# Kernel tuning notes

Hardware: AMD Instinct MI355X
Metric: run time of the kernel (lower is better)

## Reference

```python
import jax, jax.numpy as jnp
import numpy as np

B = 4096
INPUT_SIZE = 256
OUT_WINDOW = 10
C = 16
OUTPUT_SIZE = 2  # real/imag pair
WIN = INPUT_SIZE - OUT_WINDOW + 1  # 247
BN_EPS = 1e-5


def setup_inputs() -> dict:
    key = jax.random.key(0)
    ks = jax.random.split(key, 7)
    return {
        "x": jax.random.normal(ks[0], (B, INPUT_SIZE, C, 2), dtype=jnp.float32),
        "W_in_real": jax.random.normal(ks[1], (C, WIN), dtype=jnp.float32),
        "W_in_imag": jax.random.normal(ks[2], (C, WIN), dtype=jnp.float32),
        "W_nl": jax.random.normal(ks[3], (C, OUTPUT_SIZE, 2 * (C - 1)), dtype=jnp.float32) * 0.1,
        "W_coeff": jax.random.normal(ks[4], (OUTPUT_SIZE, OUTPUT_SIZE), dtype=jnp.float32),
        "W_out_real": jax.random.normal(ks[5], (C, OUT_WINDOW), dtype=jnp.float32),
        "W_out_imag": jax.random.normal(ks[6], (C, OUT_WINDOW), dtype=jnp.float32),
        "bn_gamma": jnp.ones((C,), jnp.float32),
        "bn_beta": jnp.zeros((C,), jnp.float32),
    }


def _depthwise_filter(x_bcn, w_ck):
    # per-channel valid cross-correlation: out[b,c,w] = sum_k x[b,c,w+k] * w_ck[c,k]
    kern = w_ck[:, None, :]  # (O=C, I/groups=1, K)
    return jax.lax.conv_general_dilated(
        x_bcn, kern, window_strides=(1,), padding="VALID",
        dimension_numbers=("NCH", "OIH", "NCH"), feature_group_count=C)


def reference(x, W_in_real, W_in_imag, W_nl, W_coeff, W_out_real, W_out_imag, bn_gamma, bn_beta):
    # x: [B, N, C, 2]
    x_real = jnp.transpose(x[..., 0], (0, 2, 1))  # [B, C, N]
    x_imag = jnp.transpose(x[..., 1], (0, 2, 1))
    # unfold + per-channel FIR filter == depthwise valid correlation -> [B, W, C]
    f_r = jnp.transpose(_depthwise_filter(x_real, W_in_real), (0, 2, 1))
    f_i = jnp.transpose(_depthwise_filter(x_imag, W_in_imag), (0, 2, 1))
    # cubic amplitude nonlinearity
    amp = f_r * f_r + f_i * f_i
    f_r = amp * f_r
    f_i = amp * f_i
    # masked cross-channel gather (all channels except self), static indices
    nbr = np.stack([np.delete(np.arange(C), c) for c in range(C)])  # [C, C-1]
    nonlin_in = jnp.concatenate([f_r[:, :, nbr], f_i[:, :, nbr]], axis=-1)  # [B, W, C, 2(C-1)]
    # per-channel mixing then shared coeff mix
    nonlin_out = jnp.einsum("bwcf,cof->bwco", nonlin_in, W_nl)   # [B, W, C, 2]
    coeff_out = jnp.einsum("bwco,po->bwcp", nonlin_out, W_coeff)  # [B, W, C, 2]
    # per-channel output FIR over the out_window axis
    out_r = jnp.einsum("bwc,cw->bc", coeff_out[..., 0], W_out_real)
    out_i = jnp.einsum("bwc,cw->bc", coeff_out[..., 1], W_out_imag)
    out = jnp.stack([out_r, out_i], axis=-1)  # [B, C, 2]
    # BatchNorm1d over channel axis C (training mode, biased batch stats)
    mu = jnp.mean(out, axis=(0, 2))
    var = jnp.mean(jnp.square(out - mu[None, :, None]), axis=(0, 2))
    scale = (bn_gamma * jax.lax.rsqrt(var + BN_EPS))[None, :, None]
    return (out - mu[None, :, None]) * scale + bn_beta[None, :, None]
```

## Files before the change

### kernel.cpp

```cpp
#include <hip/hip_runtime.h>

#define BTOT 4096
#define G 8
#define NC 16
#define WIN 247
#define KPAD 250
#define WST 251
#define NW 10
#define NBLK (BTOT / G)

__global__ __launch_bounds__(256) void k_main(
    const float* __restrict__ x,
    const float* __restrict__ Wr, const float* __restrict__ Wi,
    const float* __restrict__ Wnl, const float* __restrict__ Wc,
    const float* __restrict__ Wor, const float* __restrict__ Woi,
    float* __restrict__ out, float* __restrict__ ws)
{
    __shared__ float Wlds[2 * NC * WST];
    __shared__ float fbuf[G * 32 * NW];
    __shared__ float WnlS[NC * 2 * 30];
    __shared__ float WoS[2 * 160];
    __shared__ float WcS[4];
    __shared__ float red[256];
    __shared__ float redq[128];

    float* crS = Wlds;
    float* ciS = Wlds + 1280;

    const int tid = threadIdx.x;
    const int b0 = blockIdx.x * G;

    for (int idx = tid; idx < 2 * NC * KPAD; idx += 256) {
        int ri  = idx / (NC * KPAD);
        int rem = idx - ri * (NC * KPAD);
        int c   = rem / KPAD;
        int k   = rem - c * KPAD;
        float v = 0.f;
        if (k < WIN) v = ri ? Wi[c * WIN + k] : Wr[c * WIN + k];
        Wlds[ri * (NC * WST) + c * WST + k] = v;
    }
    for (int idx = tid; idx < NC * 60; idx += 256) WnlS[idx] = Wnl[idx];
    if (tid < 160) { WoS[tid] = Wor[tid]; WoS[160 + tid] = Woi[tid]; }
    if (tid < 4) WcS[tid] = Wc[tid];
    __syncthreads();

    {
        const int b_loc = tid >> 5;
        const int cri   = tid & 31;
        const int ri    = cri & 1;
        const int c     = cri >> 1;
        const float* xb = x + (size_t)(b0 + b_loc) * 8192 + cri;
        const float* Wrow = Wlds + ri * (NC * WST) + c * WST;

        float acc[NW];
        float xb10[NW];
        #pragma unroll
        for (int w = 0; w < NW; ++w) { acc[w] = 0.f; xb10[w] = xb[w * 32]; }

        for (int i0 = 0; i0 < 240; i0 += NW) {
            #pragma unroll
            for (int j = 0; j < NW; ++j) {
                float wv = Wrow[i0 + j];
                #pragma unroll
                for (int w = 0; w < NW; ++w)
                    acc[w] = fmaf(xb10[(j + w) % NW], wv, acc[w]);
                xb10[j] = xb[(i0 + j + NW) * 32];
            }
        }
        #pragma unroll
        for (int j = 0; j < NW; ++j) {
            float wv = Wrow[240 + j];
            #pragma unroll
            for (int w = 0; w < NW; ++w)
                acc[w] = fmaf(xb10[(j + w) % NW], wv, acc[w]);
            if (j < 6) xb10[j] = xb[(240 + j + NW) * 32];
        }

        #pragma unroll
        for (int w = 0; w < NW; ++w)
            fbuf[tid * NW + w] = acc[w];
    }
    __syncthreads();

    for (int idx = tid; idx < G * 160; idx += 256) {
        int b = idx / 160; int r = idx - b * 160;
        int c = r / NW;    int w = r - c * NW;
        int base = b * 320 + c * 20 + w;
        float fr = fbuf[base];
        float fi = fbuf[base + NW];
        float amp = fr * fr + fi * fi;
        fbuf[base]      = amp * fr;
        fbuf[base + NW] = amp * fi;
    }
    __syncthreads();

    for (int idx = tid; idx < G * 160; idx += 256) {
        int b = idx / 160; int r = idx - b * 160;
        int c = r / NW;    int w = r - c * NW;
        const float* f3b = fbuf + b * 320;
        const float* wn  = WnlS + c * 60;
        float s0 = 0.f, s1 = 0.f;
        #pragma unroll
        for (int j = 0; j < NC; ++j) {
            if (j != c) {
                int jj = (j > c) ? (j - 1) : j;
                float f3r = f3b[j * 20 + w];
                float f3i = f3b[j * 20 + NW + w];
                s0 += f3r * wn[jj]      + f3i * wn[15 + jj];
                s1 += f3r * wn[30 + jj] + f3i * wn[45 + jj];
            }
        }
        float p0 = s0 * WcS[0] + s1 * WcS[1];
        float p1 = s0 * WcS[2] + s1 * WcS[3];
        crS[idx] = p0 * WoS[c * NW + w];
        ciS[idx] = p1 * WoS[160 + c * NW + w];
    }
    __syncthreads();

    if (tid < G * NC) {
        int b = tid >> 4; int c = tid & 15;
        float orr = 0.f, oii = 0.f;
        #pragma unroll
        for (int w = 0; w < NW; ++w) {
            orr += crS[b * 160 + c * NW + w];
            oii += ciS[b * 160 + c * NW + w];
        }
        size_t o = ((size_t)(b0 + b) * NC + c) * 2;
        out[o]     = orr;
        out[o + 1] = oii;
        red[tid]       = orr + oii;
        redq[tid]      = orr * orr + oii * oii;
    }
    __syncthreads();
    if (tid < NC) {
        float s = 0.f, q = 0.f;
        #pragma unroll
        for (int b = 0; b < G; ++b) { s += red[b * 16 + tid]; q += redq[b * 16 + tid]; }
        ws[(tid * NBLK + blockIdx.x) * 2]     = s;
        ws[(tid * NBLK + blockIdx.x) * 2 + 1] = q;
    }
}

__global__ __launch_bounds__(256) void k_bnstat(
    const float* __restrict__ ws_in, float* __restrict__ ws_ab,
    const float* __restrict__ gamma, const float* __restrict__ beta)
{
    const int c = blockIdx.x;
    const int tid = threadIdx.x;
    float s = 0.f, q = 0.f;
    for (int i = tid; i < NBLK; i += 256) {
        s += ws_in[(c * NBLK + i) * 2];
        q += ws_in[(c * NBLK + i) * 2 + 1];
    }
    #pragma unroll
    for (int off = 32; off; off >>= 1) {
        s += __shfl_down(s, off, 64);
        q += __shfl_down(q, off, 64);
    }
    __shared__ float rs[4], rq[4];
    const int wv = tid >> 6;
    if ((tid & 63) == 0) { rs[wv] = s; rq[wv] = q; }
    __syncthreads();
    if (tid == 0) {
        s = rs[0] + rs[1] + rs[2] + rs[3];
        q = rq[0] + rq[1] + rq[2] + rq[3];
        const float inv_n = 1.f / (BTOT * 2.f);
        float mu  = s * inv_n;
        float var = q * inv_n - mu * mu;
        float sc  = gamma[c] * rsqrtf(var + 1e-5f);
        ws_ab[c]      = sc;
        ws_ab[16 + c] = beta[c] - mu * sc;
    }
}

__global__ __launch_bounds__(256) void k_bnapply(
    float* __restrict__ out, const float* __restrict__ ws_ab)
{
    __shared__ float A[16], Bb[16];
    const int tid = threadIdx.x;
    if (tid < 16) { A[tid] = ws_ab[tid]; Bb[tid] = ws_ab[16 + tid]; }
    __syncthreads();
    int idx = blockIdx.x * 256 + tid;
    if (idx < BTOT * NC * 2) {
        int c = (idx >> 1) & 15;
        out[idx] = out[idx] * A[c] + Bb[c];
    }
}

extern "C" void kernel_launch(void* const* d_in, const int* in_sizes, int n_in,
                              void* d_out, int out_size, void* d_ws, size_t ws_size,
                              hipStream_t stream)
{
    const float* x    = (const float*)d_in[0];
    const float* Wr   = (const float*)d_in[1];
    const float* Wi   = (const float*)d_in[2];
    const float* Wnl  = (const float*)d_in[3];
    const float* Wc   = (const float*)d_in[4];
    const float* Wor  = (const float*)d_in[5];
    const float* Woi  = (const float*)d_in[6];
    const float* gam  = (const float*)d_in[7];
    const float* bet  = (const float*)d_in[8];
    float* out = (float*)d_out;
    float* ws  = (float*)d_ws;
    float* ws_ab = ws + NC * NBLK * 2;

    k_main<<<NBLK, 256, 0, stream>>>(x, Wr, Wi, Wnl, Wc, Wor, Woi, out, ws);
    k_bnstat<<<NC, 256, 0, stream>>>(ws, ws_ab, gam, bet);
    k_bnapply<<<(BTOT * NC * 2 + 255) / 256, 256, 0, stream>>>(out, ws_ab);
}
```

Measured before the change: 54.00 us.

## Split FIR taps across threads with shuffle reduction and bf16-packed weights

The FIR stage is restructured so each thread handles one channel's real and imag pair over a quarter of the tap range. The x loads become float2, with a double-buffered register window, and partial sums are combined with wave shuffles. Filter weights are packed into bf16 pairs in LDS to halve the weight load traffic, and the cubic nonlinearity is folded into the FIR epilogue, removing one barrier. The batch group per block drops to 4, which doubles the block count and the weight staging per batch. Rounding the weights to bf16 loses precision against the fp32 reference.

```diff
diff --git a/kernel.cpp b/kernel.cpp
--- a/kernel.cpp
+++ b/kernel.cpp
@@ -1,13 +1,38 @@
 #include <hip/hip_runtime.h>
 
 #define BTOT 4096
-#define G 8
+#define G 4
 #define NC 16
 #define WIN 247
-#define KPAD 250
-#define WST 251
+#define KTOT 250
 #define NW 10
 #define NBLK (BTOT / G)
+
+
+__device__ __forceinline__ unsigned bf16rne(float f) {
+    unsigned u = __float_as_uint(f);
+    return (u + 0x7fffu + ((u >> 16) & 1u)) >> 16;
+}
+
+#define CHUNK(kbase, lbase, CUR, NXT, DO_LOAD)                                  \
+    _Pragma("unroll")                                                           \
+    for (int j = 0; j < 10; ++j) {                                              \
+        unsigned wp = WL[((kbase) + j) * NC + c];                               \
+        float wr = __uint_as_float(wp << 16);                                   \
+        float wi = __uint_as_float(wp & 0xffff0000u);                           \
+        _Pragma("unroll")                                                       \
+        for (int w = 0; w < 10; ++w) {                                          \
+            int idx = j + w;                                                    \
+            float2 v = (idx < 10) ? CUR[idx] : NXT[idx - 10];                   \
+            accr[w] = fmaf(v.x, wr, accr[w]);                                   \
+            acci[w] = fmaf(v.y, wi, acci[w]);                                   \
+        }                                                                       \
+        if (DO_LOAD) {                                                          \
+            int n = (lbase) + j;                                                \
+            n = (n < 255) ? n : 255;                                            \
+            CUR[j] = xp[n * 16];                                                \
+        }                                                                       \
+    }
 
 __global__ __launch_bounds__(256) void k_main(
     const float* __restrict__ x,
@@ -16,126 +41,118 @@
     const float* __restrict__ Wor, const float* __restrict__ Woi,
     float* __restrict__ out, float* __restrict__ ws)
 {
-    __shared__ float Wlds[2 * NC * WST];
-    __shared__ float fbuf[G * 32 * NW];
-    __shared__ float WnlS[NC * 2 * 30];
+    __shared__ unsigned WL[KTOT * NC];
+    __shared__ float fbuf[G * NC * 2 * NW];
+    __shared__ float WnlS[NC * 60];
     __shared__ float WoS[2 * 160];
     __shared__ float WcS[4];
-    __shared__ float red[256];
-    __shared__ float redq[128];
-
-    float* crS = Wlds;
-    float* ciS = Wlds + 1280;
+    __shared__ float crS[G * 160];
+    __shared__ float ciS[G * 160];
+    __shared__ float red[G * NC], redq[G * NC];
 
     const int tid = threadIdx.x;
-    const int b0 = blockIdx.x * G;
-
-    for (int idx = tid; idx < 2 * NC * KPAD; idx += 256) {
-        int ri  = idx / (NC * KPAD);
-        int rem = idx - ri * (NC * KPAD);
-        int c   = rem / KPAD;
-        int k   = rem - c * KPAD;
-        float v = 0.f;
-        if (k < WIN) v = ri ? Wi[c * WIN + k] : Wr[c * WIN + k];
-        Wlds[ri * (NC * WST) + c * WST + k] = v;
+    const int b   = tid >> 6;
+    const int ks  = (tid >> 4) & 3;
+    const int c   = tid & 15;
+    const int b0  = blockIdx.x * G;
+    const int k0  = ks ? (ks * 60 + 10) : 0;
+
+    const float2* xp = (const float2*)(x + (size_t)(b0 + b) * 8192) + c;
+
+    float2 bA[10], bB[10];
+    float accr[10], acci[10];
+    #pragma unroll
+    for (int j = 0; j < 10; ++j) bA[j] = xp[(k0 + j) * 16];
+    #pragma unroll
+    for (int j = 0; j < 10; ++j) bB[j] = xp[(k0 + 10 + j) * 16];
+    #pragma unroll
+    for (int w = 0; w < 10; ++w) { accr[w] = 0.f; acci[w] = 0.f; }
+
+    for (int idx = tid; idx < KTOT * NC; idx += 256) {
+        int k = idx >> 4, cc = idx & 15;
+        unsigned p = 0;
+        if (k < WIN) {
+            unsigned r = bf16rne(Wr[cc * WIN + k]);
+            unsigned i = bf16rne(Wi[cc * WIN + k]);
+            p = r | (i << 16);
+        }
+        WL[idx] = p;
     }
     for (int idx = tid; idx < NC * 60; idx += 256) WnlS[idx] = Wnl[idx];
     if (tid < 160) { WoS[tid] = Wor[tid]; WoS[160 + tid] = Woi[tid]; }
     if (tid < 4) WcS[tid] = Wc[tid];
     __syncthreads();
 
-    {
-        const int b_loc = tid >> 5;
-        const int cri   = tid & 31;
-        const int ri    = cri & 1;
-        const int c     = cri >> 1;
-        const float* xb = x + (size_t)(b0 + b_loc) * 8192 + cri;
-        const float* Wrow = Wlds + ri * (NC * WST) + c * WST;
-
-        float acc[NW];
-        float xb10[NW];
-        #pragma unroll
-        for (int w = 0; w < NW; ++w) { acc[w] = 0.f; xb10[w] = xb[w * 32]; }
-
-        for (int i0 = 0; i0 < 240; i0 += NW) {
-            #pragma unroll
-            for (int j = 0; j < NW; ++j) {
-                float wv = Wrow[i0 + j];
-                #pragma unroll
-                for (int w = 0; w < NW; ++w)
-                    acc[w] = fmaf(xb10[(j + w) % NW], wv, acc[w]);
-                xb10[j] = xb[(i0 + j + NW) * 32];
-            }
-        }
-        #pragma unroll
-        for (int j = 0; j < NW; ++j) {
-            float wv = Wrow[240 + j];
-            #pragma unroll
-            for (int w = 0; w < NW; ++w)
-                acc[w] = fmaf(xb10[(j + w) % NW], wv, acc[w]);
-            if (j < 6) xb10[j] = xb[(240 + j + NW) * 32];
-        }
-
-        #pragma unroll
-        for (int w = 0; w < NW; ++w)
-            fbuf[tid * NW + w] = acc[w];
+    CHUNK(k0 +  0, k0 + 20, bA, bB, true)
+    CHUNK(k0 + 10, k0 + 30, bB, bA, true)
+    CHUNK(k0 + 20, k0 + 40, bA, bB, true)
+    CHUNK(k0 + 30, k0 + 50, bB, bA, true)
+    CHUNK(k0 + 40, k0 + 60, bA, bB, true)
+    CHUNK(k0 + 50, k0 + 70, bB, bA, (ks == 0))
+    if (ks == 0) {
+        CHUNK(60, 0, bA, bB, false)
+    }
+
+    #pragma unroll
+    for (int w = 0; w < 10; ++w) {
+        accr[w] += __shfl_down(accr[w], 32);
+        accr[w] += __shfl_down(accr[w], 16);
+        acci[w] += __shfl_down(acci[w], 32);
+        acci[w] += __shfl_down(acci[w], 16);
+    }
+    if (ks == 0) {
+        #pragma unroll
+        for (int w = 0; w < 10; ++w) {
+            float fr = accr[w], fi = acci[w];
+            float amp = fr * fr + fi * fi;
+            fbuf[(b * NC + c) * 20 + w]      = amp * fr;
+            fbuf[(b * NC + c) * 20 + 10 + w] = amp * fi;
+        }
     }
     __syncthreads();
 
     for (int idx = tid; idx < G * 160; idx += 256) {
-        int b = idx / 160; int r = idx - b * 160;
-        int c = r / NW;    int w = r - c * NW;
-        int base = b * 320 + c * 20 + w;
-        float fr = fbuf[base];
-        float fi = fbuf[base + NW];
-        float amp = fr * fr + fi * fi;
-        fbuf[base]      = amp * fr;
-        fbuf[base + NW] = amp * fi;
-    }
-    __syncthreads();
-
-    for (int idx = tid; idx < G * 160; idx += 256) {
-        int b = idx / 160; int r = idx - b * 160;
-        int c = r / NW;    int w = r - c * NW;
-        const float* f3b = fbuf + b * 320;
-        const float* wn  = WnlS + c * 60;
+        int bb = idx / 160; int r = idx - bb * 160;
+        int cc = r / NW;    int w = r - cc * NW;
+        const float* f3 = fbuf + bb * 320;
+        const float* wn = WnlS + cc * 60;
         float s0 = 0.f, s1 = 0.f;
         #pragma unroll
         for (int j = 0; j < NC; ++j) {
-            if (j != c) {
-                int jj = (j > c) ? (j - 1) : j;
-                float f3r = f3b[j * 20 + w];
-                float f3i = f3b[j * 20 + NW + w];
+            if (j != cc) {
+                int jj = (j > cc) ? (j - 1) : j;
+                float f3r = f3[j * 20 + w];
+                float f3i = f3[j * 20 + 10 + w];
                 s0 += f3r * wn[jj]      + f3i * wn[15 + jj];
                 s1 += f3r * wn[30 + jj] + f3i * wn[45 + jj];
             }
         }
         float p0 = s0 * WcS[0] + s1 * WcS[1];
         float p1 = s0 * WcS[2] + s1 * WcS[3];
-        crS[idx] = p0 * WoS[c * NW + w];
-        ciS[idx] = p1 * WoS[160 + c * NW + w];
+        crS[idx] = p0 * WoS[cc * NW + w];
+        ciS[idx] = p1 * WoS[160 + cc * NW + w];
     }
     __syncthreads();
 
     if (tid < G * NC) {
-        int b = tid >> 4; int c = tid & 15;
+        int bb = tid >> 4; int cc = tid & 15;
         float orr = 0.f, oii = 0.f;
         #pragma unroll
         for (int w = 0; w < NW; ++w) {
-            orr += crS[b * 160 + c * NW + w];
-            oii += ciS[b * 160 + c * NW + w];
-        }
-        size_t o = ((size_t)(b0 + b) * NC + c) * 2;
+            orr += crS[bb * 160 + cc * NW + w];
+            oii += ciS[bb * 160 + cc * NW + w];
+        }
+        size_t o = ((size_t)(b0 + bb) * NC + cc) * 2;
         out[o]     = orr;
         out[o + 1] = oii;
-        red[tid]       = orr + oii;
-        redq[tid]      = orr * orr + oii * oii;
+        red[tid]  = orr + oii;
+        redq[tid] = orr * orr + oii * oii;
     }
     __syncthreads();
     if (tid < NC) {
         float s = 0.f, q = 0.f;
         #pragma unroll
-        for (int b = 0; b < G; ++b) { s += red[b * 16 + tid]; q += redq[b * 16 + tid]; }
+        for (int bb = 0; bb < G; ++bb) { s += red[bb * 16 + tid]; q += redq[bb * 16 + tid]; }
         ws[(tid * NBLK + blockIdx.x) * 2]     = s;
         ws[(tid * NBLK + blockIdx.x) * 2 + 1] = q;
     }
@@ -145,12 +162,12 @@
     const float* __restrict__ ws_in, float* __restrict__ ws_ab,
     const float* __restrict__ gamma, const float* __restrict__ beta)
 {
-    const int c = blockIdx.x;
+    const int cch = blockIdx.x;
     const int tid = threadIdx.x;
     float s = 0.f, q = 0.f;
     for (int i = tid; i < NBLK; i += 256) {
-        s += ws_in[(c * NBLK + i) * 2];
-        q += ws_in[(c * NBLK + i) * 2 + 1];
+        s += ws_in[(cch * NBLK + i) * 2];
+        q += ws_in[(cch * NBLK + i) * 2 + 1];
     }
     #pragma unroll
     for (int off = 32; off; off >>= 1) {
@@ -167,9 +184,9 @@
         const float inv_n = 1.f / (BTOT * 2.f);
         float mu  = s * inv_n;
         float var = q * inv_n - mu * mu;
-        float sc  = gamma[c] * rsqrtf(var + 1e-5f);
-        ws_ab[c]      = sc;
-        ws_ab[16 + c] = beta[c] - mu * sc;
+        float sc  = gamma[cch] * rsqrtf(var + 1e-5f);
+        ws_ab[cch]      = sc;
+        ws_ab[16 + cch] = beta[cch] - mu * sc;
     }
 }
 
@@ -182,8 +199,8 @@
     __syncthreads();
     int idx = blockIdx.x * 256 + tid;
     if (idx < BTOT * NC * 2) {
-        int c = (idx >> 1) & 15;
-        out[idx] = out[idx] * A[c] + Bb[c];
+        int cch = (idx >> 1) & 15;
+        out[idx] = out[idx] * A[cch] + Bb[cch];
     }
 }
 
```

Result: slower. 85.15 us (+57.7%).
